# Optimization experiments

Hardware: AMD Instinct MI355X
Metric: run time of the kernel (lower is better)

Reference implementation:

```python
import jax, jax.numpy as jnp
import numpy as np

D_MODEL = 1024
NUM_HEADS = 16


def setup_inputs() -> dict:
    key = jax.random.key(0)
    ks = jax.random.split(key, 5)
    B, S, D = 4, 2048, D_MODEL
    scale = 0.02  # realistic init scale so logits stay well-conditioned
    return {
        "x": jax.random.normal(ks[0], (B, S, D), dtype=jnp.float32),
        "Wq": jax.random.normal(ks[1], (D, D), dtype=jnp.float32) * scale,
        "Wk": jax.random.normal(ks[2], (D, D), dtype=jnp.float32) * scale,
        "Wv": jax.random.normal(ks[3], (D, D), dtype=jnp.float32) * scale,
        "Wo": jax.random.normal(ks[4], (D, D), dtype=jnp.float32) * scale,
    }


def reference(x, Wq, Wk, Wv, Wo):
    # x: (B, S, D). Weights are (d_out, d_in) as in the torch module.
    B, S, D = x.shape
    H = NUM_HEADS
    dk = D // H

    # Projections: einsum('oi,bli->blo') == x @ W.T
    q = jnp.einsum("oi,bsi->bso", Wq, x).reshape(B, S, H, dk).transpose(0, 2, 1, 3)
    k = jnp.einsum("oi,bsi->bso", Wk, x).reshape(B, S, H, dk).transpose(0, 2, 1, 3)
    v = jnp.einsum("oi,bsi->bso", Wv, x).reshape(B, S, H, dk).transpose(0, 2, 1, 3)

    # Scaled dot-product scores per head: (B, H, S, S)
    scores = jnp.einsum("bhqd,bhkd->bhqk", q, k) / jnp.sqrt(jnp.asarray(dk, x.dtype))

    # Causal mask (True = keep); masked entries get -inf (matches inf-subtraction)
    causal = jnp.tril(jnp.ones((S, S), dtype=bool))
    scores = jnp.where(causal, scores, -jnp.inf)

    attn = jax.nn.softmax(scores, axis=-1)

    out = jnp.einsum("bhqk,bhkd->bhqd", attn, v)  # (B, H, S, dk)
    out = out.transpose(0, 2, 1, 3).reshape(B, S, D)  # concat heads

    # Output projection: einsum('oi,bli->blo')
    return jnp.einsum("oi,bsi->bso", Wo, out)
```

## Files before the change

kernel.cpp:

```cpp
#include <hip/hip_runtime.h>
#include <hip/hip_bf16.h>

typedef unsigned short u16;
typedef __attribute__((ext_vector_type(8))) short short8;
typedef __attribute__((ext_vector_type(4))) float f32x4;

__device__ __forceinline__ float bf2f(u16 v) {
    union { unsigned u; float f; } c; c.u = ((unsigned)v) << 16; return c.f;
}
__device__ __forceinline__ u16 f2bf(float f) {
    union { float f; unsigned u; } c; c.f = f;
    unsigned r = c.u + 0x7fffu + ((c.u >> 16) & 1u);
    return (u16)(r >> 16);
}
__device__ __forceinline__ uint4 pack8(const float4 a, const float4 b) {
    uint4 r;
    r.x = (unsigned)f2bf(a.x) | ((unsigned)f2bf(a.y) << 16);
    r.y = (unsigned)f2bf(a.z) | ((unsigned)f2bf(a.w) << 16);
    r.z = (unsigned)f2bf(b.x) | ((unsigned)f2bf(b.y) << 16);
    r.w = (unsigned)f2bf(b.z) | ((unsigned)f2bf(b.w) << 16);
    return r;
}
__device__ __forceinline__ void gl_lds16(const u16* g, u16* l) {
    __builtin_amdgcn_global_load_lds((const __attribute__((address_space(1))) unsigned int*)g,
                                     (__attribute__((address_space(3))) unsigned int*)l, 16, 0, 0);
}

__global__ __launch_bounds__(256) void convert_all(const float* __restrict__ x,
                                                   const float* __restrict__ wq,
                                                   const float* __restrict__ wk,
                                                   const float* __restrict__ wv,
                                                   const float* __restrict__ wo,
                                                   u16* xb, u16* wqb, u16* wkb, u16* wvb, u16* wob) {
    size_t i8 = ((size_t)blockIdx.x * 256 + threadIdx.x) * 8;
    const float* src; u16* dst; size_t off;
    if (i8 < 8388608) { src = x; dst = xb; off = i8; }
    else {
        size_t idx = i8 - 8388608;
        int w = (int)(idx >> 20); off = idx & 1048575;
        src = (w == 0) ? wq : (w == 1) ? wk : (w == 2) ? wv : wo;
        dst = (w == 0) ? wqb : (w == 1) ? wkb : (w == 2) ? wvb : wob;
    }
    float4 a = *(const float4*)&src[off];
    float4 b = *(const float4*)&src[off + 4];
    *(uint4*)&dst[off] = pack8(a, b);
}

__device__ __forceinline__ void gemm_core(const u16* __restrict__ A, const u16* __restrict__ B,
                                          int m0, int n0, u16* As, u16* Bs, f32x4 acc[4][4]) {
    const int tid = threadIdx.x;
    const int wv = tid >> 6, lane = tid & 63, lr = lane & 15, quad = lane >> 4;
    const int srow = lane >> 3;
    const int scg  = (lane & 7) ^ srow;
    const int wm = (wv >> 1) * 64, wn = (wv & 1) * 64;

    for (int kt = 0; kt < 1024; kt += 64) {
        __syncthreads();
        #pragma unroll
        for (int t = 0; t < 4; ++t) {
            int r = wv * 32 + t * 8;
            gl_lds16(&A[(size_t)(m0 + r + srow) * 1024 + kt + scg * 8], &As[r * 64]);
            gl_lds16(&B[(size_t)(n0 + r + srow) * 1024 + kt + scg * 8], &Bs[r * 64]);
        }
        __syncthreads();
        #pragma unroll
        for (int c = 0; c < 2; ++c) {
            short8 af[4], bf[4];
            #pragma unroll
            for (int mi = 0; mi < 4; ++mi)
                af[mi] = *(const short8*)&As[(wm + mi * 16 + lr) * 64 + (((c * 4 + quad) ^ (lr & 7)) * 8)];
            #pragma unroll
            for (int ni = 0; ni < 4; ++ni)
                bf[ni] = *(const short8*)&Bs[(wn + ni * 16 + lr) * 64 + (((c * 4 + quad) ^ (lr & 7)) * 8)];
            #pragma unroll
            for (int mi = 0; mi < 4; ++mi)
                #pragma unroll
                for (int ni = 0; ni < 4; ++ni)
                    acc[mi][ni] = __builtin_amdgcn_mfma_f32_16x16x32_bf16(af[mi], bf[ni], acc[mi][ni], 0, 0, 0);
        }
    }
}

__global__ __launch_bounds__(256) void gemm_qkv(const u16* __restrict__ xb,
                                                const u16* __restrict__ wq,
                                                const u16* __restrict__ wk,
                                                const u16* __restrict__ wv,
                                                u16* __restrict__ Qb, u16* __restrict__ Kb,
                                                u16* __restrict__ Vtb) {
    __shared__ __align__(16) u16 As[8192];
    __shared__ __align__(16) u16 Bs[8192];
    const int z = blockIdx.z;
    const u16* A; const u16* B; int m0, n0;
    if (z == 2) { A = wv; B = xb; m0 = blockIdx.x * 128; n0 = blockIdx.y * 128; }
    else        { A = xb; B = (z ? wk : wq); m0 = blockIdx.y * 128; n0 = blockIdx.x * 128; }

    f32x4 acc[4][4];
    #pragma unroll
    for (int i = 0; i < 4; ++i)
        #pragma unroll
        for (int j = 0; j < 4; ++j) acc[i][j] = 0;

    gemm_core(A, B, m0, n0, As, Bs, acc);

    const int lane = threadIdx.x & 63, lr = lane & 15, quad = lane >> 4;
    const int wv4 = threadIdx.x >> 6;
    const int wm = (wv4 >> 1) * 64, wn = (wv4 & 1) * 64;
    const float scale = (z == 0) ? 0.18033688f : 1.0f;
    #pragma unroll
    for (int mi = 0; mi < 4; ++mi)
        #pragma unroll
        for (int ni = 0; ni < 4; ++ni)
            #pragma unroll
            for (int reg = 0; reg < 4; ++reg) {
                int row = m0 + wm + mi * 16 + quad * 4 + reg;
                int col = n0 + wn + ni * 16 + lr;
                u16 bv = f2bf(acc[mi][ni][reg] * scale);
                if (z == 2) {
                    int bhh = (col >> 11) * 16 + (row >> 6);
                    Vtb[(size_t)bhh * 131072 + (size_t)(row & 63) * 2048 + (col & 2047)] = bv;
                } else {
                    int bhh = (row >> 11) * 16 + (col >> 6);
                    (z ? Kb : Qb)[(size_t)bhh * 131072 + (size_t)(row & 2047) * 64 + (col & 63)] = bv;
                }
            }
}

__global__ __launch_bounds__(256) void gemm_out(const u16* __restrict__ Ob,
                                                const u16* __restrict__ wo,
                                                float* __restrict__ C) {
    __shared__ __align__(16) u16 As[8192];
    __shared__ __align__(16) u16 Bs[8192];
    const int m0 = blockIdx.y * 128, n0 = blockIdx.x * 128;

    f32x4 acc[4][4];
    #pragma unroll
    for (int i = 0; i < 4; ++i)
        #pragma unroll
        for (int j = 0; j < 4; ++j) acc[i][j] = 0;

    gemm_core(Ob, wo, m0, n0, As, Bs, acc);

    const int lane = threadIdx.x & 63, lr = lane & 15, quad = lane >> 4;
    const int wv4 = threadIdx.x >> 6;
    const int wm = (wv4 >> 1) * 64, wn = (wv4 & 1) * 64;
    #pragma unroll
    for (int mi = 0; mi < 4; ++mi)
        #pragma unroll
        for (int ni = 0; ni < 4; ++ni)
            #pragma unroll
            for (int reg = 0; reg < 4; ++reg) {
                int row = m0 + wm + mi * 16 + quad * 4 + reg;
                int col = n0 + wn + ni * 16 + lr;
                C[(size_t)row * 1024 + col] = acc[mi][ni][reg];
            }
}

__global__ __launch_bounds__(256) void attn_flash(const u16* __restrict__ Q,
                                                  const u16* __restrict__ K,
                                                  const u16* __restrict__ Vt,
                                                  u16* __restrict__ O) {
    __shared__ __align__(16) u16 Kbuf[2][4096];
    __shared__ __align__(16) u16 Vbuf[2][4096];
    __shared__ __align__(16) u16 Ps[4][2048];

    const int tid = threadIdx.x, wave = tid >> 6, lane = tid & 63;
    const int lr = lane & 15, quad = lane >> 4;
    const int bh = blockIdx.x & 63;
    const int qt = 15 - (blockIdx.x >> 6);
    const int qbase = qt * 128 + wave * 32;
    const size_t base = (size_t)bh * 131072;

    const int srow = lane >> 3;
    const int scg  = (lane & 7) ^ srow;

    short8 qf[2][2];
    #pragma unroll
    for (int qmi = 0; qmi < 2; ++qmi)
        #pragma unroll
        for (int c = 0; c < 2; ++c)
            qf[qmi][c] = *(const short8*)&Q[base + (size_t)(qbase + qmi * 16 + lr) * 64 + c * 32 + quad * 8];

    float l_r[2] = {0.f, 0.f};
    f32x4 oacc[4][2];
    #pragma unroll
    for (int i = 0; i < 4; ++i) { oacc[i][0] = 0; oacc[i][1] = 0; }

    const int jmax = 2 * qt + 1;

    #pragma unroll
    for (int t = 0; t < 2; ++t) {
        int r0 = wave * 16 + t * 8;
        gl_lds16(&K[base + (size_t)(r0 + srow) * 64 + scg * 8], &Kbuf[0][r0 * 64]);
        gl_lds16(&Vt[base + (size_t)(r0 + srow) * 2048 + scg * 8], &Vbuf[0][r0 * 64]);
    }

    for (int j = 0; j <= jmax; ++j) {
        const int buf = j & 1;
        __syncthreads();
        if (j < jmax) {
            const int nb = buf ^ 1;
            #pragma unroll
            for (int t = 0; t < 2; ++t) {
                int r0 = wave * 16 + t * 8;
                gl_lds16(&K[base + (size_t)((j + 1) * 64 + r0 + srow) * 64 + scg * 8], &Kbuf[nb][r0 * 64]);
                gl_lds16(&Vt[base + (size_t)(r0 + srow) * 2048 + (j + 1) * 64 + scg * 8], &Vbuf[nb][r0 * 64]);
            }
        }

        if (j * 64 <= qbase + 31) {
            f32x4 st[4][2];
            #pragma unroll
            for (int ni = 0; ni < 4; ++ni) { st[ni][0] = 0; st[ni][1] = 0; }
            #pragma unroll
            for (int c = 0; c < 2; ++c) {
                short8 kf[4];
                #pragma unroll
                for (int ni = 0; ni < 4; ++ni)
                    kf[ni] = *(const short8*)&Kbuf[buf][(ni * 16 + lr) * 64 + (((c * 4 + quad) ^ (lr & 7)) * 8)];
                #pragma unroll
                for (int ni = 0; ni < 4; ++ni)
                    #pragma unroll
                    for (int qmi = 0; qmi < 2; ++qmi)
                        st[ni][qmi] = __builtin_amdgcn_mfma_f32_16x16x32_bf16(kf[ni], qf[qmi][c], st[ni][qmi], 0, 0, 0);
            }

            if (j >= 2 * qt) {
                #pragma unroll
                for (int ni = 0; ni < 4; ++ni)
                    #pragma unroll
                    for (int qmi = 0; qmi < 2; ++qmi)
                        #pragma unroll
                        for (int reg = 0; reg < 4; ++reg) {
                            int key = j * 64 + ni * 16 + quad * 4 + reg;
                            int q   = qbase + qmi * 16 + lr;
                            if (key > q) st[ni][qmi][reg] = -3.0e38f;
                        }
            }

            #pragma unroll
            for (int qmi = 0; qmi < 2; ++qmi) {
                float rs = 0.f;
                #pragma unroll
                for (int ni = 0; ni < 4; ++ni) {
                    unsigned u0 = __float_as_uint(exp2f(st[ni][qmi][0]));
                    unsigned u1 = __float_as_uint(exp2f(st[ni][qmi][1]));
                    unsigned u2 = __float_as_uint(exp2f(st[ni][qmi][2]));
                    unsigned u3 = __float_as_uint(exp2f(st[ni][qmi][3]));
                    rs += __uint_as_float(u0 & 0xffff0000u) + __uint_as_float(u1 & 0xffff0000u)
                        + __uint_as_float(u2 & 0xffff0000u) + __uint_as_float(u3 & 0xffff0000u);
                    uint2 pk;
                    pk.x = __builtin_amdgcn_perm(u1, u0, 0x07060302);
                    pk.y = __builtin_amdgcn_perm(u3, u2, 0x07060302);
                    int g8 = ni * 2 + (quad >> 1);
                    *(uint2*)&Ps[wave][qmi * 1024 + lr * 64 + ((g8 ^ (lr & 7)) * 8 + (quad & 1) * 4)] = pk;
                }
                l_r[qmi] += rs;
            }

            #pragma unroll
            for (int c = 0; c < 2; ++c) {
                short8 pf[2];
                #pragma unroll
                for (int qmi = 0; qmi < 2; ++qmi)
                    pf[qmi] = *(const short8*)&Ps[wave][qmi * 1024 + lr * 64 + (((c * 4 + quad) ^ (lr & 7)) * 8)];
                #pragma unroll
                for (int dmi = 0; dmi < 4; ++dmi) {
                    short8 vf = *(const short8*)&Vbuf[buf][(dmi * 16 + lr) * 64 + (((c * 4 + quad) ^ (lr & 7)) * 8)];
                    #pragma unroll
                    for (int qmi = 0; qmi < 2; ++qmi)
                        oacc[dmi][qmi] = __builtin_amdgcn_mfma_f32_16x16x32_bf16(vf, pf[qmi], oacc[dmi][qmi], 0, 0, 0);
                }
            }
        }
    }

    const int b = bh >> 4, h = bh & 15;
    #pragma unroll
    for (int qmi = 0; qmi < 2; ++qmi) {
        float l = l_r[qmi];
        l += __shfl_xor(l, 16, 64);
        l += __shfl_xor(l, 32, 64);
        float rl = 1.0f / l;
        int s = qbase + qmi * 16 + lr;
        #pragma unroll
        for (int dmi = 0; dmi < 4; ++dmi) {
            unsigned o0 = f2bf(oacc[dmi][qmi][0] * rl);
            unsigned o1 = f2bf(oacc[dmi][qmi][1] * rl);
            unsigned o2 = f2bf(oacc[dmi][qmi][2] * rl);
            unsigned o3 = f2bf(oacc[dmi][qmi][3] * rl);
            uint2 pk;
            pk.x = o0 | (o1 << 16);
            pk.y = o2 | (o3 << 16);
            *(uint2*)&O[((size_t)(b * 2048 + s)) * 1024 + h * 64 + dmi * 16 + quad * 4] = pk;
        }
    }
}

extern "C" void kernel_launch(void* const* d_in, const int* in_sizes, int n_in,
                              void* d_out, int out_size, void* d_ws, size_t ws_size,
                              hipStream_t stream) {
    const float* x  = (const float*)d_in[0];
    const float* Wq = (const float*)d_in[1];
    const float* Wk = (const float*)d_in[2];
    const float* Wv = (const float*)d_in[3];
    const float* Wo = (const float*)d_in[4];

    u16* xb  = (u16*)d_ws;
    u16* wqb = xb + 8388608;
    u16* wkb = wqb + 1048576;
    u16* wvb = wkb + 1048576;
    u16* wob = wvb + 1048576;
    u16* Qb  = wob + 1048576;
    u16* Kb  = Qb + 8388608;
    u16* Vtb = Kb + 8388608;
    u16* Ob  = xb;

    convert_all<<<6144, 256, 0, stream>>>(x, Wq, Wk, Wv, Wo, xb, wqb, wkb, wvb, wob);

    gemm_qkv<<<dim3(8, 64, 3), 256, 0, stream>>>(xb, wqb, wkb, wvb, Qb, Kb, Vtb);

    attn_flash<<<1024, 256, 0, stream>>>(Qb, Kb, Vtb, Ob);

    gemm_out<<<dim3(8, 64), 256, 0, stream>>>(Ob, wob, (float*)d_out);
}
```

Measured before the change: 261.0 us.

## Use 512-thread attention blocks covering 256 queries and compute row sums via MFMA

Each attention block now runs 8 waves over 256 query rows, so each K/V tile loaded into LDS is shared by twice as many waves and each wave loads only one 8-row slice. The query-tile order is reshuffled so heavy and light causal tiles are mixed across the grid. The softmax denominator is now accumulated by an extra MFMA against a ones vector rather than with scalar adds and cross-lane shuffles. Larger blocks mean fewer blocks and coarser causal work imbalance, and there is a higher LDS and register footprint per block.

```diff
diff --git a/kernel.cpp b/kernel.cpp
--- a/kernel.cpp
+++ b/kernel.cpp
@@ -155,24 +155,27 @@
             }
 }
 
-__global__ __launch_bounds__(256) void attn_flash(const u16* __restrict__ Q,
-                                                  const u16* __restrict__ K,
-                                                  const u16* __restrict__ Vt,
-                                                  u16* __restrict__ O) {
+__global__ __launch_bounds__(512, 4) void attn_flash(const u16* __restrict__ Q,
+                                                     const u16* __restrict__ K,
+                                                     const u16* __restrict__ Vt,
+                                                     u16* __restrict__ O) {
     __shared__ __align__(16) u16 Kbuf[2][4096];
     __shared__ __align__(16) u16 Vbuf[2][4096];
-    __shared__ __align__(16) u16 Ps[4][2048];
+    __shared__ __align__(16) u16 Ps[8][2048];
 
     const int tid = threadIdx.x, wave = tid >> 6, lane = tid & 63;
     const int lr = lane & 15, quad = lane >> 4;
     const int bh = blockIdx.x & 63;
-    const int qt = 15 - (blockIdx.x >> 6);
-    const int qbase = qt * 128 + wave * 32;
+    const int p  = blockIdx.x >> 6;
+    const int qt8 = (p < 4) ? (7 - p) : (p - 4);
+    const int qbase = qt8 * 256 + wave * 32;
     const size_t base = (size_t)bh * 131072;
 
     const int srow = lane >> 3;
     const int scg  = (lane & 7) ^ srow;
 
+    const short8 onesv = {0x3f80, 0x3f80, 0x3f80, 0x3f80, 0x3f80, 0x3f80, 0x3f80, 0x3f80};
+
     short8 qf[2][2];
     #pragma unroll
     for (int qmi = 0; qmi < 2; ++qmi)
@@ -180,31 +183,25 @@
         for (int c = 0; c < 2; ++c)
             qf[qmi][c] = *(const short8*)&Q[base + (size_t)(qbase + qmi * 16 + lr) * 64 + c * 32 + quad * 8];
 
-    float l_r[2] = {0.f, 0.f};
     f32x4 oacc[4][2];
     #pragma unroll
     for (int i = 0; i < 4; ++i) { oacc[i][0] = 0; oacc[i][1] = 0; }
-
-    const int jmax = 2 * qt + 1;
-
-    #pragma unroll
-    for (int t = 0; t < 2; ++t) {
-        int r0 = wave * 16 + t * 8;
-        gl_lds16(&K[base + (size_t)(r0 + srow) * 64 + scg * 8], &Kbuf[0][r0 * 64]);
-        gl_lds16(&Vt[base + (size_t)(r0 + srow) * 2048 + scg * 8], &Vbuf[0][r0 * 64]);
-    }
+    f32x4 lacc[2];
+    lacc[0] = 0; lacc[1] = 0;
+
+    const int jmax = 4 * qt8 + 3;
+    const int r0 = wave * 8;
+
+    gl_lds16(&K[base + (size_t)(r0 + srow) * 64 + scg * 8], &Kbuf[0][r0 * 64]);
+    gl_lds16(&Vt[base + (size_t)(r0 + srow) * 2048 + scg * 8], &Vbuf[0][r0 * 64]);
 
     for (int j = 0; j <= jmax; ++j) {
         const int buf = j & 1;
         __syncthreads();
         if (j < jmax) {
             const int nb = buf ^ 1;
-            #pragma unroll
-            for (int t = 0; t < 2; ++t) {
-                int r0 = wave * 16 + t * 8;
-                gl_lds16(&K[base + (size_t)((j + 1) * 64 + r0 + srow) * 64 + scg * 8], &Kbuf[nb][r0 * 64]);
-                gl_lds16(&Vt[base + (size_t)(r0 + srow) * 2048 + (j + 1) * 64 + scg * 8], &Vbuf[nb][r0 * 64]);
-            }
+            gl_lds16(&K[base + (size_t)((j + 1) * 64 + r0 + srow) * 64 + scg * 8], &Kbuf[nb][r0 * 64]);
+            gl_lds16(&Vt[base + (size_t)(r0 + srow) * 2048 + (j + 1) * 64 + scg * 8], &Vbuf[nb][r0 * 64]);
         }
 
         if (j * 64 <= qbase + 31) {
@@ -224,7 +221,7 @@
                         st[ni][qmi] = __builtin_amdgcn_mfma_f32_16x16x32_bf16(kf[ni], qf[qmi][c], st[ni][qmi], 0, 0, 0);
             }
 
-            if (j >= 2 * qt) {
+            if (j >= 4 * qt8) {
                 #pragma unroll
                 for (int ni = 0; ni < 4; ++ni)
                     #pragma unroll
@@ -239,22 +236,18 @@
 
             #pragma unroll
             for (int qmi = 0; qmi < 2; ++qmi) {
-                float rs = 0.f;
                 #pragma unroll
                 for (int ni = 0; ni < 4; ++ni) {
                     unsigned u0 = __float_as_uint(exp2f(st[ni][qmi][0]));
                     unsigned u1 = __float_as_uint(exp2f(st[ni][qmi][1]));
                     unsigned u2 = __float_as_uint(exp2f(st[ni][qmi][2]));
                     unsigned u3 = __float_as_uint(exp2f(st[ni][qmi][3]));
-                    rs += __uint_as_float(u0 & 0xffff0000u) + __uint_as_float(u1 & 0xffff0000u)
-                        + __uint_as_float(u2 & 0xffff0000u) + __uint_as_float(u3 & 0xffff0000u);
                     uint2 pk;
                     pk.x = __builtin_amdgcn_perm(u1, u0, 0x07060302);
                     pk.y = __builtin_amdgcn_perm(u3, u2, 0x07060302);
                     int g8 = ni * 2 + (quad >> 1);
                     *(uint2*)&Ps[wave][qmi * 1024 + lr * 64 + ((g8 ^ (lr & 7)) * 8 + (quad & 1) * 4)] = pk;
                 }
-                l_r[qmi] += rs;
             }
 
             #pragma unroll
@@ -270,6 +263,9 @@
                     for (int qmi = 0; qmi < 2; ++qmi)
                         oacc[dmi][qmi] = __builtin_amdgcn_mfma_f32_16x16x32_bf16(vf, pf[qmi], oacc[dmi][qmi], 0, 0, 0);
                 }
+                #pragma unroll
+                for (int qmi = 0; qmi < 2; ++qmi)
+                    lacc[qmi] = __builtin_amdgcn_mfma_f32_16x16x32_bf16(onesv, pf[qmi], lacc[qmi], 0, 0, 0);
             }
         }
     }
@@ -277,10 +273,7 @@
     const int b = bh >> 4, h = bh & 15;
     #pragma unroll
     for (int qmi = 0; qmi < 2; ++qmi) {
-        float l = l_r[qmi];
-        l += __shfl_xor(l, 16, 64);
-        l += __shfl_xor(l, 32, 64);
-        float rl = 1.0f / l;
+        float rl = 1.0f / lacc[qmi][0];
         int s = qbase + qmi * 16 + lr;
         #pragma unroll
         for (int dmi = 0; dmi < 4; ++dmi) {
@@ -319,7 +312,7 @@
 
     gemm_qkv<<<dim3(8, 64, 3), 256, 0, stream>>>(xb, wqb, wkb, wvb, Qb, Kb, Vtb);
 
-    attn_flash<<<1024, 256, 0, stream>>>(Qb, Kb, Vtb, Ob);
+    attn_flash<<<512, 512, 0, stream>>>(Qb, Kb, Vtb, Ob);
 
     gemm_out<<<dim3(8, 64), 256, 0, stream>>>(Ob, wob, (float*)d_out);
 }
```

Measured after the change: 260.7 us. About the same (-0.1%).
